# Kernel tuning notes

Hardware: AMD Instinct MI355X
Metric: run time of the kernel (lower is better)

The kernel has to match this reference:

```python
import jax, jax.numpy as jnp
import numpy as np

EPS = 1e-07
BETA = 1.0
NEG_INF = -1e30


def setup_inputs() -> dict:
    key = jax.random.key(0)
    k1, k2 = jax.random.split(key)
    B, C = 262144, 128
    inputs = jax.random.normal(k1, (B, C), dtype=jnp.float32)
    targets = jax.random.randint(k2, (B,), 0, C, dtype=jnp.int64)
    return {"inputs": inputs, "targets": targets}


def reference(inputs, targets):
    B, C = inputs.shape
    dt = inputs.dtype
    probs = jax.nn.sigmoid(inputs)  # (B, C)

    # per-class counts (size_class in torch code)
    counts = jax.ops.segment_sum(jnp.ones((B,), dtype=dt), targets, num_segments=C)  # (C,)
    present = counts > 0
    safe_counts = jnp.where(present, counts, jnp.asarray(1.0, dt))

    # per-class mean of probs over samples with that label -> rows of mean_probs
    sum_probs = jax.ops.segment_sum(probs, targets, num_segments=C)  # (C, C)
    mean_probs = sum_probs / safe_counts[:, None]
    diag = jnp.arange(C)
    mean_probs = mean_probs.at[diag, diag].set(-1.0)  # mean_probs_k[k] = -1

    # positive term: mean over class-k samples of log(p[i,k]+eps), summed over present classes
    logp_pos_true = jnp.log(jnp.take_along_axis(probs, targets[:, None], axis=1)[:, 0] + EPS)  # (B,)
    pos_per_class = jax.ops.segment_sum(logp_pos_true, targets, num_segments=C) / safe_counts
    loss_pos = jnp.sum(jnp.where(present, pos_per_class, jnp.asarray(0.0, dt)))

    # per-class mean of log(1-p+eps) with the true-class column zeroed ((1-onehot) factor)
    logp_neg = jnp.log(1.0 - probs + EPS)  # (B, C)
    sum_logneg = jax.ops.segment_sum(logp_neg, targets, num_segments=C)  # (C, C)
    mean_loss_neg = (sum_logneg / safe_counts[:, None]).at[diag, diag].set(0.0)

    # negative term: per column k, softmax over present rows j != k of beta*mean_probs[j,k]
    mask = present[:, None] & (~jnp.eye(C, dtype=bool))  # rows j, cols k
    logits = jnp.where(mask, BETA * mean_probs, jnp.asarray(NEG_INF, dt))
    weights = jax.nn.softmax(logits, axis=0) * mask.astype(dt)  # zero weight when column fully masked
    loss_neg = jnp.sum(weights * mean_loss_neg)

    return -1.0 * (loss_pos + loss_neg)
```

## Files before the change

### kernel.cpp

```cpp
#include <hip/hip_runtime.h>
#include <math.h>

#define C      128
#define CAPLG  12
#define CAP    (1 << CAPLG)
#define SPLIT  16
#define NMB    (C * SPLIT)
#define SPB    1024
#define CSTR   16
#define PBS    260
#define LN2F   0.69314718056f

__device__ __forceinline__ float fast_rcp(float x) { return __builtin_amdgcn_rcpf(x); }

__global__ __launch_bounds__(256)
void scatter_kernel(const int* __restrict__ tgt, int* __restrict__ cursor2,
                    int* __restrict__ perm, int B) {
    __shared__ int lcur[C];
    __shared__ int sbase[C];
    if (threadIdx.x < C) lcur[threadIdx.x] = 0;
    __syncthreads();
    const int base = blockIdx.x * SPB + threadIdx.x * 4;
    int t0 = -1, t1 = -1, t2 = -1, t3 = -1;
    if (base + 3 < B) {
        int4 t4 = *reinterpret_cast<const int4*>(tgt + base);
        t0 = t4.x; t1 = t4.y; t2 = t4.z; t3 = t4.w;
    } else {
        if (base     < B) t0 = tgt[base];
        if (base + 1 < B) t1 = tgt[base + 1];
        if (base + 2 < B) t2 = tgt[base + 2];
        if (base + 3 < B) t3 = tgt[base + 3];
    }
    int r0 = (t0 >= 0) ? atomicAdd(&lcur[t0], 1) : 0;
    int r1 = (t1 >= 0) ? atomicAdd(&lcur[t1], 1) : 0;
    int r2 = (t2 >= 0) ? atomicAdd(&lcur[t2], 1) : 0;
    int r3 = (t3 >= 0) ? atomicAdd(&lcur[t3], 1) : 0;
    __syncthreads();
    if (threadIdx.x < C)
        sbase[threadIdx.x] = atomicAdd(&cursor2[threadIdx.x * CSTR], lcur[threadIdx.x]);
    __syncthreads();
    if (t0 >= 0) perm[(t0 << CAPLG) + sbase[t0] + r0] = base;
    if (t1 >= 0) perm[(t1 << CAPLG) + sbase[t1] + r1] = base + 1;
    if (t2 >= 0) perm[(t2 << CAPLG) + sbase[t2] + r2] = base + 2;
    if (t3 >= 0) perm[(t3 << CAPLG) + sbase[t3] + r3] = base + 3;
}

__global__ __launch_bounds__(256)
void main_kernel(const float* __restrict__ x, const int* __restrict__ perm,
                 const int* __restrict__ cursor2, float* __restrict__ partial) {
    const int k = blockIdx.x >> 4;
    const int p = blockIdx.x & (SPLIT - 1);
    const int n = min(cursor2[k * CSTR], CAP);
    const int chunk = (n + SPLIT - 1) >> 4;
    const int s0 = min(p * chunk, n);
    const int s1 = min(s0 + chunk, n);

    const int tid  = threadIdx.x;
    const int wave = tid >> 6;
    const int lane = tid & 63;
    const bool poslane = (lane == (k >> 1));
    const int  kpar = k & 1;

    const int wlen = (s1 - s0 + 3) >> 2;
    const int ws0  = s0 + wave * wlen;
    const int ws1  = min(ws0 + wlen, s1);
    const int wn   = (ws1 > ws0) ? (ws1 - ws0) : 0;

    const int* bperm = perm + (k << CAPLG);
    const int pv = (lane < wn) ? bperm[ws0 + lane] : 0;

    float ap0 = 0.f, ap1 = 0.f, sx0 = 0.f, sx1 = 0.f, sl0 = 0.f, sl1 = 0.f;
    float apos = 0.f;

    if (wn > 0) {
        const float* xl = x + 2 * lane;
        float2 b0 = *reinterpret_cast<const float2*>(xl + (size_t)__shfl(pv, 0) * C);
        float2 b1 = *reinterpret_cast<const float2*>(xl + (size_t)__shfl(pv, min(1, wn - 1)) * C);
        float2 b2 = *reinterpret_cast<const float2*>(xl + (size_t)__shfl(pv, min(2, wn - 1)) * C);
        for (int j = 0; j < wn; ++j) {
            float2 cur = b0; b0 = b1; b1 = b2;
            if (j + 3 < wn)
                b2 = *reinterpret_cast<const float2*>(xl + (size_t)__shfl(pv, j + 3) * C);
            float e0 = __expf(-cur.x), u0 = 1.f + e0, l0 = __log2f(u0);
            float e1 = __expf(-cur.y), u1 = 1.f + e1, l1 = __log2f(u1);
            ap0 += fast_rcp(u0); sx0 += cur.x; sl0 += l0;
            ap1 += fast_rcp(u1); sx1 += cur.y; sl1 += l1;
            if (poslane) apos += kpar ? l1 : l0;
        }
    }

    __shared__ __align__(8) float sP[4][C];
    __shared__ __align__(8) float sX[4][C];
    __shared__ __align__(8) float sL[4][C];
    __shared__ float sPos[4];
    *reinterpret_cast<float2*>(&sP[wave][2 * lane]) = make_float2(ap0, ap1);
    *reinterpret_cast<float2*>(&sX[wave][2 * lane]) = make_float2(sx0, sx1);
    *reinterpret_cast<float2*>(&sL[wave][2 * lane]) = make_float2(sl0, sl1);
    if (poslane) sPos[wave] = apos;
    __syncthreads();

    float* mine = partial + (size_t)blockIdx.x * PBS;
    if (tid < C) {
        mine[tid] = sP[0][tid] + sP[1][tid] + sP[2][tid] + sP[3][tid];
    } else {
        const int t = tid - C;
        float sx = sX[0][t] + sX[1][t] + sX[2][t] + sX[3][t];
        float sl = sL[0][t] + sL[1][t] + sL[2][t] + sL[3][t];
        mine[C + t] = -sx - LN2F * sl;
    }
    if (tid == 0)
        mine[256] = -LN2F * (sPos[0] + sPos[1] + sPos[2] + sPos[3]);
}

__global__ __launch_bounds__(128)
void finalize_kernel(const float* __restrict__ partial, const int* __restrict__ cursor2,
                     float* __restrict__ colpart, int* __restrict__ ticket,
                     float* __restrict__ out) {
    const int k   = blockIdx.x;
    const int tid = threadIdx.x;

    __shared__ float spcol[C], slcol[C];
    __shared__ float sposr[SPLIT];

    {
        const int j = tid;
        const float* rowp = partial + (size_t)j * SPLIT * PBS;
        float aP = 0.f, aL = 0.f;
#pragma unroll
        for (int q = 0; q < SPLIT; ++q) {
            aP += rowp[q * PBS + k];
            aL += rowp[q * PBS + C + k];
        }
        spcol[j] = aP; slcol[j] = aL;
        if (tid < SPLIT)
            sposr[tid] = partial[((size_t)k * SPLIT + tid) * PBS + 256];
    }
    __syncthreads();

    if (tid < 64) {
        const int l = tid, j0 = l, j1 = l + 64;
        const float c0 = (float)cursor2[j0 * CSTR];
        const float c1 = (float)cursor2[j1 * CSTR];
        const bool  v0 = (j0 != k) && (c0 > 0.f);
        const bool  v1 = (j1 != k) && (c1 > 0.f);
        const float x0 = v0 ? spcol[j0] / c0 : -INFINITY;
        const float x1 = v1 ? spcol[j1] / c1 : -INFINITY;

        float m = fmaxf(x0, x1);
#pragma unroll
        for (int d = 1; d < 64; d <<= 1) m = fmaxf(m, __shfl_xor(m, d));

        float w0 = v0 ? __expf(x0 - m) : 0.f;
        float w1 = v1 ? __expf(x1 - m) : 0.f;
        float den = w0 + w1;
        float num = (v0 ? w0 * (slcol[j0] / c0) : 0.f)
                  + (v1 ? w1 * (slcol[j1] / c1) : 0.f);
#pragma unroll
        for (int d = 1; d < 64; d <<= 1) { den += __shfl_xor(den, d); num += __shfl_xor(num, d); }

        int last = 0;
        if (l == 0) {
            float colneg = (den > 0.f) ? num / den : 0.f;
            float ck     = (float)cursor2[k * CSTR];
            float ps     = 0.f;
#pragma unroll
            for (int q = 0; q < SPLIT; ++q) ps += sposr[q];
            float pk = (ck > 0.f) ? ps / ck : 0.f;
            colpart[k] = colneg + pk;
            __threadfence();
            last = (atomicAdd(ticket, 1) == C - 1);
        }
        last = __shfl(last, 0);
        if (last) {
            __threadfence();
            float s = colpart[l] + colpart[l + 64];
#pragma unroll
            for (int d = 1; d < 64; d <<= 1) s += __shfl_xor(s, d);
            if (l == 0) out[0] = -s;
        }
    }
}

extern "C" void kernel_launch(void* const* d_in, const int* in_sizes, int n_in,
                              void* d_out, int out_size, void* d_ws, size_t ws_size,
                              hipStream_t stream) {
    const float* x   = (const float*)d_in[0];
    const int*   tgt = (const int*)d_in[1];
    const int B = in_sizes[1];

    int*   cursor2 = (int*)d_ws;
    int*   ticket  = cursor2 + C * CSTR;
    int*   perm    = cursor2 + C * CSTR + CSTR;
    float* partial = (float*)(perm + C * CAP);
    float* colpart = partial + (size_t)NMB * PBS;

    hipMemsetAsync(cursor2, 0, (C * CSTR + CSTR) * sizeof(int), stream);
    scatter_kernel<<<(B + SPB - 1) / SPB, 256, 0, stream>>>(tgt, cursor2, perm, B);
    main_kernel<<<NMB, 256, 0, stream>>>(x, perm, cursor2, partial);
    finalize_kernel<<<C, 128, 0, stream>>>(partial, cursor2, colpart, ticket, (float*)d_out);
}
```

Baseline: 51.51 us.

## Replace scatter/gather segment sums with bf16 MFMA one-hot matmul accumulation

The per-class segment sums are now computed as one-hot(targets)^T times probabilities and log(1-p) tiles using bf16 MFMA instructions over row tiles streamed in order. This removes the scatter/permutation pass and the random-row gathers. A persistent grid of 256 blocks double-buffers tiles in LDS, then a separate reduce kernel sums the per-block partials before finalize. The change trades fp32 precision for bf16 in the matmul operands, clamps log values, and adds a large partial-buffer reduction step. The ticket counter is now reset inside the reduce kernel instead of by a memset.

```diff
diff --git a/kernel.cpp b/kernel.cpp
--- a/kernel.cpp
+++ b/kernel.cpp
@@ -1,146 +1,201 @@
 #include <hip/hip_runtime.h>
 #include <math.h>
 
-#define C      128
-#define CAPLG  12
-#define CAP    (1 << CAPLG)
-#define SPLIT  16
-#define NMB    (C * SPLIT)
-#define SPB    1024
-#define CSTR   16
-#define PBS    260
-#define LN2F   0.69314718056f
+#define C        128
+#define TPB      512
+#define NB       256
+#define PSTRIDE  33024
+#define LOFF     16384
+#define POSOFF   32768
+#define CNTOFF   32896
+#define LN2F     0.6931471805599453f
+
+typedef __attribute__((ext_vector_type(8))) short bf16x8;
+typedef __attribute__((ext_vector_type(4))) float f32x4;
 
 __device__ __forceinline__ float fast_rcp(float x) { return __builtin_amdgcn_rcpf(x); }
 
+__device__ __forceinline__ unsigned f2bf(float f) {
+    unsigned u = __builtin_bit_cast(unsigned, f);
+    return (u + 0x7FFFu + ((u >> 16) & 1u)) >> 16;
+}
+
+__device__ __forceinline__ bf16x8 ld_frag(const unsigned short* s) {
+    uint2 a = *reinterpret_cast<const uint2*>(s);
+    uint2 b = *reinterpret_cast<const uint2*>(s + 4);
+    uint4 u = make_uint4(a.x, a.y, b.x, b.y);
+    return __builtin_bit_cast(bf16x8, u);
+}
+
+__global__ __launch_bounds__(TPB, 2)
+void mfma_main(const float* __restrict__ x, const int* __restrict__ tgt,
+               float* __restrict__ partial, int ntiles) {
+    const int tid = threadIdx.x;
+    const int c   = tid & 127;
+    const int q   = tid >> 7;
+    const int w   = tid >> 6;
+    const int l   = tid & 63;
+    const int g   = l >> 4;
+    const int l15 = l & 15;
+    const int wq  = w >> 2;
+    const int wr  = w & 3;
+
+    __shared__ __align__(16) unsigned short PbS[2][128 * 36];
+    __shared__ __align__(16) unsigned short LbS[2][128 * 36];
+    __shared__ __align__(16) unsigned short B3aS[2][36];
+    __shared__ __align__(16) unsigned short B3bS[2][36];
+    __shared__ __align__(16) int            TgS[2][32];
+
+    f32x4 accP[4][2], accL[4][2], acc3[4];
+#pragma unroll
+    for (int i = 0; i < 4; ++i) {
+#pragma unroll
+        for (int j = 0; j < 2; ++j) {
+            accP[i][j] = (f32x4){0.f, 0.f, 0.f, 0.f};
+            accL[i][j] = (f32x4){0.f, 0.f, 0.f, 0.f};
+        }
+        acc3[i] = (f32x4){0.f, 0.f, 0.f, 0.f};
+    }
+
+    int   r0 = blockIdx.x * 32;
+    float xv[8]; int tkv[8]; int tks = 0;
+#pragma unroll
+    for (int j = 0; j < 8; ++j) {
+        xv[j]  = x[(r0 + 8 * q + j) * C + c];
+        tkv[j] = tgt[r0 + 8 * q + j];
+    }
+    if (tid < 32) tks = tgt[r0 + tid];
+
+    int p = 0;
+    for (int t = blockIdx.x; t < ntiles; t += NB) {
+        unsigned short* Pb = PbS[p];
+        unsigned short* Lb = LbS[p];
+#pragma unroll
+        for (int jp = 0; jp < 4; ++jp) {
+            const int j0 = 2 * jp;
+            float v0 = xv[j0], v1 = xv[j0 + 1];
+            float e0 = __expf(-v0), e1 = __expf(-v1);
+            float u0 = 1.f + e0,    u1 = 1.f + e1;
+            float lu0 = __log2f(u0), lu1 = __log2f(u1);
+            float p0 = fast_rcp(u0), p1 = fast_rcp(u1);
+            float lq0 = fmaxf(fmaf(-LN2F, lu0, -v0), -16.118f);
+            float lq1 = fmaxf(fmaf(-LN2F, lu1, -v1), -16.118f);
+            const int sb = (((2 * q + (jp >> 1)) & 3) << 3) + ((q >> 1) << 2) + ((jp & 1) << 1);
+            *reinterpret_cast<unsigned*>(&Pb[c * 36 + sb]) = f2bf(p0)  | (f2bf(p1)  << 16);
+            *reinterpret_cast<unsigned*>(&Lb[c * 36 + sb]) = f2bf(lq0) | (f2bf(lq1) << 16);
+            if (c == tkv[j0])     B3aS[p][sb]     = (unsigned short)f2bf(fminf(lu0, 23.25f));
+            if (c == tkv[j0 + 1]) B3aS[p][sb + 1] = (unsigned short)f2bf(fminf(lu1, 23.25f));
+            if (c == 0) *reinterpret_cast<unsigned*>(&B3bS[p][sb]) = 0x3F803F80u;
+        }
+        if (tid < 32)
+            TgS[p][(((tid >> 2) & 3) << 3) + ((tid >> 4) << 2) + (tid & 3)] = tks;
+
+        const bool hn = (t + NB) < ntiles;
+        const int  rn = hn ? (t + NB) * 32 : r0;
+        float xn[8]; int tn[8];
+#pragma unroll
+        for (int j = 0; j < 8; ++j) {
+            xn[j] = x[(rn + 8 * q + j) * C + c];
+            tn[j] = tgt[rn + 8 * q + j];
+        }
+        const int tns = (tid < 32) ? tgt[rn + tid] : 0;
+
+        __syncthreads();
+
+        const int4* tg = reinterpret_cast<const int4*>(&TgS[p][g * 8]);
+        const int4 ta = tg[0], tb = tg[1];
+        bf16x8 afr[4];
+#pragma unroll
+        for (int i = 0; i < 4; ++i) {
+            const int cls = wq * 64 + i * 16 + l15;
+            unsigned w0 = ((ta.x == cls) ? 0x3F80u : 0u) | (((ta.y == cls) ? 0x3F80u : 0u) << 16);
+            unsigned w1 = ((ta.z == cls) ? 0x3F80u : 0u) | (((ta.w == cls) ? 0x3F80u : 0u) << 16);
+            unsigned w2 = ((tb.x == cls) ? 0x3F80u : 0u) | (((tb.y == cls) ? 0x3F80u : 0u) << 16);
+            unsigned w3 = ((tb.z == cls) ? 0x3F80u : 0u) | (((tb.w == cls) ? 0x3F80u : 0u) << 16);
+            afr[i] = __builtin_bit_cast(bf16x8, make_uint4(w0, w1, w2, w3));
+        }
+#pragma unroll
+        for (int jj = 0; jj < 2; ++jj) {
+            const int col = (wr * 2 + jj) * 16 + l15;
+            const bf16x8 bp = ld_frag(&PbS[p][col * 36 + g * 8]);
+            const bf16x8 bl = ld_frag(&LbS[p][col * 36 + g * 8]);
+#pragma unroll
+            for (int i = 0; i < 4; ++i) {
+                accP[i][jj] = __builtin_amdgcn_mfma_f32_16x16x32_bf16(afr[i], bp, accP[i][jj], 0, 0, 0);
+                accL[i][jj] = __builtin_amdgcn_mfma_f32_16x16x32_bf16(afr[i], bl, accL[i][jj], 0, 0, 0);
+            }
+        }
+        if (wr == 0) {
+            const uint4 ua = __builtin_bit_cast(uint4, ld_frag(&B3aS[p][g * 8]));
+            const uint4 ub = __builtin_bit_cast(uint4, ld_frag(&B3bS[p][g * 8]));
+            const uint4 us = (l15 == 0) ? ua : ((l15 == 1) ? ub : make_uint4(0u, 0u, 0u, 0u));
+            const bf16x8 b3 = __builtin_bit_cast(bf16x8, us);
+#pragma unroll
+            for (int i = 0; i < 4; ++i)
+                acc3[i] = __builtin_amdgcn_mfma_f32_16x16x32_bf16(afr[i], b3, acc3[i], 0, 0, 0);
+        }
+
+#pragma unroll
+        for (int j = 0; j < 8; ++j) { xv[j] = xn[j]; tkv[j] = tn[j]; }
+        tks = tns;
+        r0  = rn;
+        p  ^= 1;
+    }
+
+    float* mp = partial + (size_t)blockIdx.x * PSTRIDE;
+#pragma unroll
+    for (int i = 0; i < 4; ++i) {
+#pragma unroll
+        for (int jj = 0; jj < 2; ++jj) {
+            const int col = (wr * 2 + jj) * 16 + l15;
+#pragma unroll
+            for (int r = 0; r < 4; ++r) {
+                const int row = wq * 64 + i * 16 + g * 4 + r;
+                mp[row * C + col]        = accP[i][jj][r];
+                mp[LOFF + row * C + col] = accL[i][jj][r];
+            }
+        }
+        if (wr == 0) {
+#pragma unroll
+            for (int r = 0; r < 4; ++r) {
+                const int row = wq * 64 + i * 16 + g * 4 + r;
+                if (l15 == 0) mp[POSOFF + row] = acc3[i][r];
+                if (l15 == 1) mp[CNTOFF + row] = acc3[i][r];
+            }
+        }
+    }
+}
+
 __global__ __launch_bounds__(256)
-void scatter_kernel(const int* __restrict__ tgt, int* __restrict__ cursor2,
-                    int* __restrict__ perm, int B) {
-    __shared__ int lcur[C];
-    __shared__ int sbase[C];
-    if (threadIdx.x < C) lcur[threadIdx.x] = 0;
-    __syncthreads();
-    const int base = blockIdx.x * SPB + threadIdx.x * 4;
-    int t0 = -1, t1 = -1, t2 = -1, t3 = -1;
-    if (base + 3 < B) {
-        int4 t4 = *reinterpret_cast<const int4*>(tgt + base);
-        t0 = t4.x; t1 = t4.y; t2 = t4.z; t3 = t4.w;
-    } else {
-        if (base     < B) t0 = tgt[base];
-        if (base + 1 < B) t1 = tgt[base + 1];
-        if (base + 2 < B) t2 = tgt[base + 2];
-        if (base + 3 < B) t3 = tgt[base + 3];
-    }
-    int r0 = (t0 >= 0) ? atomicAdd(&lcur[t0], 1) : 0;
-    int r1 = (t1 >= 0) ? atomicAdd(&lcur[t1], 1) : 0;
-    int r2 = (t2 >= 0) ? atomicAdd(&lcur[t2], 1) : 0;
-    int r3 = (t3 >= 0) ? atomicAdd(&lcur[t3], 1) : 0;
-    __syncthreads();
-    if (threadIdx.x < C)
-        sbase[threadIdx.x] = atomicAdd(&cursor2[threadIdx.x * CSTR], lcur[threadIdx.x]);
-    __syncthreads();
-    if (t0 >= 0) perm[(t0 << CAPLG) + sbase[t0] + r0] = base;
-    if (t1 >= 0) perm[(t1 << CAPLG) + sbase[t1] + r1] = base + 1;
-    if (t2 >= 0) perm[(t2 << CAPLG) + sbase[t2] + r2] = base + 2;
-    if (t3 >= 0) perm[(t3 << CAPLG) + sbase[t3] + r3] = base + 3;
-}
-
-__global__ __launch_bounds__(256)
-void main_kernel(const float* __restrict__ x, const int* __restrict__ perm,
-                 const int* __restrict__ cursor2, float* __restrict__ partial) {
-    const int k = blockIdx.x >> 4;
-    const int p = blockIdx.x & (SPLIT - 1);
-    const int n = min(cursor2[k * CSTR], CAP);
-    const int chunk = (n + SPLIT - 1) >> 4;
-    const int s0 = min(p * chunk, n);
-    const int s1 = min(s0 + chunk, n);
-
-    const int tid  = threadIdx.x;
-    const int wave = tid >> 6;
-    const int lane = tid & 63;
-    const bool poslane = (lane == (k >> 1));
-    const int  kpar = k & 1;
-
-    const int wlen = (s1 - s0 + 3) >> 2;
-    const int ws0  = s0 + wave * wlen;
-    const int ws1  = min(ws0 + wlen, s1);
-    const int wn   = (ws1 > ws0) ? (ws1 - ws0) : 0;
-
-    const int* bperm = perm + (k << CAPLG);
-    const int pv = (lane < wn) ? bperm[ws0 + lane] : 0;
-
-    float ap0 = 0.f, ap1 = 0.f, sx0 = 0.f, sx1 = 0.f, sl0 = 0.f, sl1 = 0.f;
-    float apos = 0.f;
-
-    if (wn > 0) {
-        const float* xl = x + 2 * lane;
-        float2 b0 = *reinterpret_cast<const float2*>(xl + (size_t)__shfl(pv, 0) * C);
-        float2 b1 = *reinterpret_cast<const float2*>(xl + (size_t)__shfl(pv, min(1, wn - 1)) * C);
-        float2 b2 = *reinterpret_cast<const float2*>(xl + (size_t)__shfl(pv, min(2, wn - 1)) * C);
-        for (int j = 0; j < wn; ++j) {
-            float2 cur = b0; b0 = b1; b1 = b2;
-            if (j + 3 < wn)
-                b2 = *reinterpret_cast<const float2*>(xl + (size_t)__shfl(pv, j + 3) * C);
-            float e0 = __expf(-cur.x), u0 = 1.f + e0, l0 = __log2f(u0);
-            float e1 = __expf(-cur.y), u1 = 1.f + e1, l1 = __log2f(u1);
-            ap0 += fast_rcp(u0); sx0 += cur.x; sl0 += l0;
-            ap1 += fast_rcp(u1); sx1 += cur.y; sl1 += l1;
-            if (poslane) apos += kpar ? l1 : l0;
-        }
-    }
-
-    __shared__ __align__(8) float sP[4][C];
-    __shared__ __align__(8) float sX[4][C];
-    __shared__ __align__(8) float sL[4][C];
-    __shared__ float sPos[4];
-    *reinterpret_cast<float2*>(&sP[wave][2 * lane]) = make_float2(ap0, ap1);
-    *reinterpret_cast<float2*>(&sX[wave][2 * lane]) = make_float2(sx0, sx1);
-    *reinterpret_cast<float2*>(&sL[wave][2 * lane]) = make_float2(sl0, sl1);
-    if (poslane) sPos[wave] = apos;
-    __syncthreads();
-
-    float* mine = partial + (size_t)blockIdx.x * PBS;
-    if (tid < C) {
-        mine[tid] = sP[0][tid] + sP[1][tid] + sP[2][tid] + sP[3][tid];
-    } else {
-        const int t = tid - C;
-        float sx = sX[0][t] + sX[1][t] + sX[2][t] + sX[3][t];
-        float sl = sL[0][t] + sL[1][t] + sL[2][t] + sL[3][t];
-        mine[C + t] = -sx - LN2F * sl;
-    }
-    if (tid == 0)
-        mine[256] = -LN2F * (sPos[0] + sPos[1] + sPos[2] + sPos[3]);
+void reduce_kernel(const float* __restrict__ partial, float* __restrict__ red,
+                   int* __restrict__ ticket) {
+    const int e = blockIdx.x * 256 + threadIdx.x;
+    const float* pp = partial + e;
+    float s0 = 0.f, s1 = 0.f, s2 = 0.f, s3 = 0.f;
+    for (int b = 0; b < NB; b += 4) {
+        s0 += pp[(size_t)(b    ) * PSTRIDE];
+        s1 += pp[(size_t)(b + 1) * PSTRIDE];
+        s2 += pp[(size_t)(b + 2) * PSTRIDE];
+        s3 += pp[(size_t)(b + 3) * PSTRIDE];
+    }
+    red[e] = (s0 + s1) + (s2 + s3);
+    if (e == 0) *ticket = 0;
 }
 
 __global__ __launch_bounds__(128)
-void finalize_kernel(const float* __restrict__ partial, const int* __restrict__ cursor2,
-                     float* __restrict__ colpart, int* __restrict__ ticket,
-                     float* __restrict__ out) {
-    const int k   = blockIdx.x;
+void finalize_kernel(const float* __restrict__ red, float* __restrict__ colpart,
+                     int* __restrict__ ticket, float* __restrict__ out) {
+    const int k = blockIdx.x;
     const int tid = threadIdx.x;
-
-    __shared__ float spcol[C], slcol[C];
-    __shared__ float sposr[SPLIT];
-
-    {
-        const int j = tid;
-        const float* rowp = partial + (size_t)j * SPLIT * PBS;
-        float aP = 0.f, aL = 0.f;
-#pragma unroll
-        for (int q = 0; q < SPLIT; ++q) {
-            aP += rowp[q * PBS + k];
-            aL += rowp[q * PBS + C + k];
-        }
-        spcol[j] = aP; slcol[j] = aL;
-        if (tid < SPLIT)
-            sposr[tid] = partial[((size_t)k * SPLIT + tid) * PBS + 256];
-    }
+    __shared__ float spcol[C], slcol[C], scnt[C];
+    spcol[tid] = red[tid * C + k];
+    slcol[tid] = red[LOFF + tid * C + k];
+    scnt[tid]  = red[CNTOFF + tid];
     __syncthreads();
 
     if (tid < 64) {
         const int l = tid, j0 = l, j1 = l + 64;
-        const float c0 = (float)cursor2[j0 * CSTR];
-        const float c1 = (float)cursor2[j1 * CSTR];
+        const float c0 = scnt[j0], c1 = scnt[j1];
         const bool  v0 = (j0 != k) && (c0 > 0.f);
         const bool  v1 = (j1 != k) && (c1 > 0.f);
         const float x0 = v0 ? spcol[j0] / c0 : -INFINITY;
@@ -149,7 +204,6 @@
         float m = fmaxf(x0, x1);
 #pragma unroll
         for (int d = 1; d < 64; d <<= 1) m = fmaxf(m, __shfl_xor(m, d));
-
         float w0 = v0 ? __expf(x0 - m) : 0.f;
         float w1 = v1 ? __expf(x1 - m) : 0.f;
         float den = w0 + w1;
@@ -161,11 +215,8 @@
         int last = 0;
         if (l == 0) {
             float colneg = (den > 0.f) ? num / den : 0.f;
-            float ck     = (float)cursor2[k * CSTR];
-            float ps     = 0.f;
-#pragma unroll
-            for (int q = 0; q < SPLIT; ++q) ps += sposr[q];
-            float pk = (ck > 0.f) ? ps / ck : 0.f;
+            float ck = scnt[k];
+            float pk = (ck > 0.f) ? (-LN2F) * red[POSOFF + k] / ck : 0.f;
             colpart[k] = colneg + pk;
             __threadfence();
             last = (atomicAdd(ticket, 1) == C - 1);
@@ -187,15 +238,14 @@
     const float* x   = (const float*)d_in[0];
     const int*   tgt = (const int*)d_in[1];
     const int B = in_sizes[1];
-
-    int*   cursor2 = (int*)d_ws;
-    int*   ticket  = cursor2 + C * CSTR;
-    int*   perm    = cursor2 + C * CSTR + CSTR;
-    float* partial = (float*)(perm + C * CAP);
-    float* colpart = partial + (size_t)NMB * PBS;
-
-    hipMemsetAsync(cursor2, 0, (C * CSTR + CSTR) * sizeof(int), stream);
-    scatter_kernel<<<(B + SPB - 1) / SPB, 256, 0, stream>>>(tgt, cursor2, perm, B);
-    main_kernel<<<NMB, 256, 0, stream>>>(x, perm, cursor2, partial);
-    finalize_kernel<<<C, 128, 0, stream>>>(partial, cursor2, colpart, ticket, (float*)d_out);
-}
+    const int ntiles = B >> 5;
+
+    float* partial = (float*)d_ws;
+    float* red     = partial + (size_t)NB * PSTRIDE;
+    float* colpart = red + PSTRIDE;
+    int*   ticket  = (int*)(colpart + C);
+
+    mfma_main<<<NB, TPB, 0, stream>>>(x, tgt, partial, ntiles);
+    reduce_kernel<<<PSTRIDE / 256, 256, 0, stream>>>(partial, red, ticket);
+    finalize_kernel<<<C, 128, 0, stream>>>(red, colpart, ticket, (float*)d_out);
+}
```

Result: slower. 90.13 us (+75.0%).
